# Kernel tuning notes

Measured on AMD Instinct MI355X. Metric: run time of the kernel, lower is better.

The kernel has to match this reference:

```python
import jax, jax.numpy as jnp
import numpy as np

B, D_IN, D_H = 8192, 1024, 1024

def setup_inputs() -> dict:
    key = jax.random.key(0)
    ks = jax.random.split(key, 20)
    s_in = 1.0 / np.sqrt(D_IN)
    s_h = 1.0 / np.sqrt(D_H)
    inp = {
        'input': jax.random.normal(ks[0], (B, D_IN), jnp.float32),
        'h_0': jax.random.normal(ks[1], (B, D_H), jnp.float32),
        'c_0': jax.random.normal(ks[2], (B, D_H), jnp.float32),
    }
    names = ['i', 'f', 'g', 'o']
    for idx, g in enumerate(names):
        inp[f'W_{g}_i2h'] = jax.random.uniform(ks[3 + 4 * idx], (D_H, D_IN), jnp.float32, -s_in, s_in)
        inp[f'b_{g}_i2h'] = jax.random.uniform(ks[4 + 4 * idx], (D_H,), jnp.float32, -s_in, s_in)
        inp[f'W_{g}_h2h'] = jax.random.uniform(ks[5 + 4 * idx], (D_H, D_H), jnp.float32, -s_h, s_h)
        inp[f'b_{g}_h2h'] = jax.random.uniform(ks[6 + 4 * idx], (D_H,), jnp.float32, -s_h, s_h)
    return inp


def reference(input, h_0, c_0,
              W_i_i2h, b_i_i2h, W_i_h2h, b_i_h2h,
              W_f_i2h, b_f_i2h, W_f_h2h, b_f_h2h,
              W_g_i2h, b_g_i2h, W_g_h2h, b_g_h2h,
              W_o_i2h, b_o_i2h, W_o_h2h, b_o_h2h):
    # pre-activations: x @ W_i2h^T + b + h @ W_h2h^T + b  (Linear uses y = x W^T + b)
    def lin(x, W, b):
        return x @ W.T + b
    it = jax.nn.sigmoid(lin(input, W_i_i2h, b_i_i2h) + lin(h_0, W_i_h2h, b_i_h2h))
    ft = jax.nn.sigmoid(lin(input, W_f_i2h, b_f_i2h) + lin(h_0, W_f_h2h, b_f_h2h))
    ot = jax.nn.sigmoid(lin(input, W_o_i2h, b_o_i2h) + lin(h_0, W_o_h2h, b_o_h2h))
    gt = jnp.tanh(lin(input, W_g_i2h, b_g_i2h) + lin(h_0, W_g_h2h, b_g_h2h))
    ct = ft * c_0 + it * gt
    output = ot * jnp.tanh(ct)
    return (output, ct)
```

## Files before the change

### kernel.cpp

```cpp
#include <hip/hip_runtime.h>
#include <cstdint>

typedef __attribute__((ext_vector_type(8))) short bf16x8;
typedef __attribute__((ext_vector_type(4))) float f32x4;
typedef __attribute__((ext_vector_type(4))) unsigned short u16x4;
typedef __attribute__((ext_vector_type(8))) unsigned short u16x8;

typedef __attribute__((address_space(1))) unsigned int gu32_t;
typedef __attribute__((address_space(3))) unsigned int lu32_t;

#define BATCH 8192
#define DIN 1024
#define DH 1024
#define KD 2048
#define ND 4096

__device__ __forceinline__ unsigned short f2bf(float f) {
    union { float f; unsigned int u; } v; v.f = f;
    unsigned int u = v.u;
    u += 0x7fffu + ((u >> 16) & 1u);
    return (unsigned short)(u >> 16);
}
__device__ __forceinline__ float bf2f(unsigned short s) {
    union { unsigned int u; float f; } v; v.u = ((unsigned int)s) << 16;
    return v.f;
}
__device__ __forceinline__ float sigmoidf_(float x) {
    return 1.0f / (1.0f + __expf(-x));
}
__device__ __forceinline__ float tanhf_(float x) {
    float xc = fminf(fmaxf(x, -15.0f), 15.0f);
    float e2 = __expf(2.0f * xc);
    return (e2 - 1.0f) / (e2 + 1.0f);
}

__global__ void __launch_bounds__(256) convert_A(const float* __restrict__ x,
                                                 const float* __restrict__ h,
                                                 unsigned short* __restrict__ A) {
    const int t = blockIdx.x * 256 + threadIdx.x;
    const int64_t off = (int64_t)t * 8;
    const int row = (int)(off >> 11);
    const int k = (int)(off & 2047);
    const float* src = (k < DIN) ? (x + (int64_t)row * DIN + k)
                                 : (h + (int64_t)row * DH + (k - DIN));
    f32x4 v0 = *(const f32x4*)src;
    f32x4 v1 = *(const f32x4*)(src + 4);
    u16x8 o;
    o[0] = f2bf(v0[0]); o[1] = f2bf(v0[1]); o[2] = f2bf(v0[2]); o[3] = f2bf(v0[3]);
    o[4] = f2bf(v1[0]); o[5] = f2bf(v1[1]); o[6] = f2bf(v1[2]); o[7] = f2bf(v1[3]);
    *(u16x8*)(A + off) = o;
}

__global__ void __launch_bounds__(256) convert_B(
        const float* __restrict__ Wii, const float* __restrict__ Wih,
        const float* __restrict__ Wfi, const float* __restrict__ Wfh,
        const float* __restrict__ Wgi, const float* __restrict__ Wgh,
        const float* __restrict__ Woi, const float* __restrict__ Woh,
        unsigned short* __restrict__ B) {
    const int t = blockIdx.x * 256 + threadIdx.x;
    const int64_t off = (int64_t)t * 8;
    const int brow = (int)(off >> 11);
    const int k = (int)(off & 2047);
    const int gate = brow >> 10;
    const int n = brow & 1023;
    const float* Wi2h = (gate == 0) ? Wii : (gate == 1) ? Wfi : (gate == 2) ? Wgi : Woi;
    const float* Wh2h = (gate == 0) ? Wih : (gate == 1) ? Wfh : (gate == 2) ? Wgh : Woh;
    const float* src = (k < 1024) ? (Wi2h + (int64_t)n * 1024 + k)
                                  : (Wh2h + (int64_t)n * 1024 + (k - 1024));
    f32x4 v0 = *(const f32x4*)src;
    f32x4 v1 = *(const f32x4*)(src + 4);
    u16x8 o;
    o[0] = f2bf(v0[0]); o[1] = f2bf(v0[1]); o[2] = f2bf(v0[2]); o[3] = f2bf(v0[3]);
    o[4] = f2bf(v1[0]); o[5] = f2bf(v1[1]); o[6] = f2bf(v1[2]); o[7] = f2bf(v1[3]);
    *(u16x8*)(B + off) = o;
}

__global__ void __launch_bounds__(256) gemm_preact(
        const unsigned short* __restrict__ A,
        const unsigned short* __restrict__ Bw,
        unsigned short* __restrict__ C) {
    __shared__ __align__(16) unsigned short ldsA[128 * 32];
    __shared__ __align__(16) unsigned short ldsB[128 * 32];

    const int bid = blockIdx.x;
    const int swz = ((bid & 7) << 8) | (bid >> 3);
    const int bm = swz >> 5;
    const int bn = swz & 31;
    const int t = threadIdx.x;
    const int lane = t & 63;
    const int wave = t >> 6;
    const int wm = (wave >> 1) << 6;
    const int wn = (wave & 1) << 6;

    f32x4 acc[4][4];
#pragma unroll
    for (int m = 0; m < 4; ++m)
#pragma unroll
        for (int n = 0; n < 4; ++n)
            acc[m][n] = (f32x4){0.f, 0.f, 0.f, 0.f};

    const int c0i = t;
    const int c1i = t + 256;
    const int64_t aOff0 = (int64_t)(bm * 128 + (c0i >> 2)) * KD + ((c0i & 3) << 3);
    const int64_t aOff1 = (int64_t)(bm * 128 + (c1i >> 2)) * KD + ((c1i & 3) << 3);
    const int64_t bOff0 = (int64_t)(bn * 128 + (c0i >> 2)) * KD + ((c0i & 3) << 3);
    const int64_t bOff1 = (int64_t)(bn * 128 + (c1i >> 2)) * KD + ((c1i & 3) << 3);
    unsigned short* lA0 = &ldsA[wave * 512];
    unsigned short* lA1 = &ldsA[2048 + wave * 512];
    unsigned short* lB0 = &ldsB[wave * 512];
    unsigned short* lB1 = &ldsB[2048 + wave * 512];

    const int r = lane & 15;
    const int kq = (lane >> 4) << 3;

    for (int k0 = 0; k0 < KD; k0 += 32) {
        __syncthreads();
        __builtin_amdgcn_global_load_lds((const gu32_t*)(A + aOff0 + k0), (lu32_t*)lA0, 16, 0, 0);
        __builtin_amdgcn_global_load_lds((const gu32_t*)(A + aOff1 + k0), (lu32_t*)lA1, 16, 0, 0);
        __builtin_amdgcn_global_load_lds((const gu32_t*)(Bw + bOff0 + k0), (lu32_t*)lB0, 16, 0, 0);
        __builtin_amdgcn_global_load_lds((const gu32_t*)(Bw + bOff1 + k0), (lu32_t*)lB1, 16, 0, 0);
        __syncthreads();

        bf16x8 af[4], bfr[4];
#pragma unroll
        for (int m = 0; m < 4; ++m)
            af[m] = *(const bf16x8*)&ldsA[(wm + m * 16 + r) * 32 + kq];
#pragma unroll
        for (int n = 0; n < 4; ++n)
            bfr[n] = *(const bf16x8*)&ldsB[(wn + n * 16 + r) * 32 + kq];
#pragma unroll
        for (int m = 0; m < 4; ++m)
#pragma unroll
            for (int n = 0; n < 4; ++n)
                acc[m][n] = __builtin_amdgcn_mfma_f32_16x16x32_bf16(af[m], bfr[n], acc[m][n], 0, 0, 0);
    }

    const int colBase = bn * 128 + wn + r;
    const int rowBase = bm * 128 + wm + ((lane >> 4) << 2);
#pragma unroll
    for (int m = 0; m < 4; ++m)
#pragma unroll
        for (int n = 0; n < 4; ++n) {
            const int col = colBase + n * 16;
#pragma unroll
            for (int j = 0; j < 4; ++j) {
                const int row = rowBase + m * 16 + j;
                C[(int64_t)row * ND + col] = f2bf(acc[m][n][j]);
            }
        }
}

__global__ void __launch_bounds__(256) lstm_epilogue(
        const unsigned short* __restrict__ C,
        const float* __restrict__ c0,
        const float* __restrict__ bii, const float* __restrict__ bih,
        const float* __restrict__ bfi, const float* __restrict__ bfh,
        const float* __restrict__ bgi, const float* __restrict__ bgh,
        const float* __restrict__ boi, const float* __restrict__ boh,
        float* __restrict__ out) {
    const int t = blockIdx.x * 256 + threadIdx.x;
    const int64_t e = (int64_t)t * 4;
    const int n = (int)(e & 1023);
    const int64_t cb = ((e >> 10) << 12) | n;
    u16x4 pi = *(const u16x4*)&C[cb];
    u16x4 pf = *(const u16x4*)&C[cb + 1024];
    u16x4 pg = *(const u16x4*)&C[cb + 2048];
    u16x4 po = *(const u16x4*)&C[cb + 3072];
    f32x4 cv = *(const f32x4*)&c0[e];
    f32x4 b_i0 = *(const f32x4*)&bii[n], b_i1 = *(const f32x4*)&bih[n];
    f32x4 b_f0 = *(const f32x4*)&bfi[n], b_f1 = *(const f32x4*)&bfh[n];
    f32x4 b_g0 = *(const f32x4*)&bgi[n], b_g1 = *(const f32x4*)&bgh[n];
    f32x4 b_o0 = *(const f32x4*)&boi[n], b_o1 = *(const f32x4*)&boh[n];
    f32x4 ov, ctv;
#pragma unroll
    for (int j = 0; j < 4; ++j) {
        float it = sigmoidf_(bf2f(pi[j]) + b_i0[j] + b_i1[j]);
        float ft = sigmoidf_(bf2f(pf[j]) + b_f0[j] + b_f1[j]);
        float gt = tanhf_(bf2f(pg[j]) + b_g0[j] + b_g1[j]);
        float ot = sigmoidf_(bf2f(po[j]) + b_o0[j] + b_o1[j]);
        float ct = ft * cv[j] + it * gt;
        ctv[j] = ct;
        ov[j] = ot * tanhf_(ct);
    }
    *(f32x4*)&out[e] = ov;
    *(f32x4*)&out[(int64_t)BATCH * DH + e] = ctv;
}

extern "C" void kernel_launch(void* const* d_in, const int* in_sizes, int n_in,
                              void* d_out, int out_size, void* d_ws, size_t ws_size,
                              hipStream_t stream) {
    const float* x   = (const float*)d_in[0];
    const float* h0  = (const float*)d_in[1];
    const float* c0  = (const float*)d_in[2];
    const float* Wii = (const float*)d_in[3];
    const float* bii = (const float*)d_in[4];
    const float* Wih = (const float*)d_in[5];
    const float* bih = (const float*)d_in[6];
    const float* Wfi = (const float*)d_in[7];
    const float* bfi = (const float*)d_in[8];
    const float* Wfh = (const float*)d_in[9];
    const float* bfh = (const float*)d_in[10];
    const float* Wgi = (const float*)d_in[11];
    const float* bgi = (const float*)d_in[12];
    const float* Wgh = (const float*)d_in[13];
    const float* bgh = (const float*)d_in[14];
    const float* Woi = (const float*)d_in[15];
    const float* boi = (const float*)d_in[16];
    const float* Woh = (const float*)d_in[17];
    const float* boh = (const float*)d_in[18];

    unsigned short* A  = (unsigned short*)d_ws;
    unsigned short* Bw = A + (size_t)BATCH * KD;
    unsigned short* C  = Bw + (size_t)ND * KD;
    float* out = (float*)d_out;

    convert_A<<<8192, 256, 0, stream>>>(x, h0, A);
    convert_B<<<4096, 256, 0, stream>>>(Wii, Wih, Wfi, Wfh, Wgi, Wgh, Woi, Woh, Bw);
    gemm_preact<<<2048, 256, 0, stream>>>(A, Bw, C);
    lstm_epilogue<<<8192, 256, 0, stream>>>(C, c0, bii, bih, bfi, bfh, bgi, bgh, boi, boh, out);
}
```

Baseline: 379.1 us.

## Fuse LSTM epilogue into GEMM with gate-interleaved weights and merged conversion kernel

Weight rows are reordered so the four gates for each hidden unit sit next to each other in N. Each GEMM tile can then compute the LSTM cell directly, staging its accumulators through LDS and writing h and c without the bf16 preactivation buffer. The two conversion kernels are merged into one that also precomputes summed biases, cutting launches and the round trip of an 8192x4096 intermediate. The cost is an added LDS-staged epilogue with extra barriers and more LDS per block, which may lower occupancy.

After: 406.5 us. 1.07x slower.

```diff
diff --git a/kernel.cpp b/kernel.cpp
--- a/kernel.cpp
+++ b/kernel.cpp
@@ -3,7 +3,6 @@
 
 typedef __attribute__((ext_vector_type(8))) short bf16x8;
 typedef __attribute__((ext_vector_type(4))) float f32x4;
-typedef __attribute__((ext_vector_type(4))) unsigned short u16x4;
 typedef __attribute__((ext_vector_type(8))) unsigned short u16x8;
 
 typedef __attribute__((address_space(1))) unsigned int gu32_t;
@@ -21,10 +20,6 @@
     u += 0x7fffu + ((u >> 16) & 1u);
     return (unsigned short)(u >> 16);
 }
-__device__ __forceinline__ float bf2f(unsigned short s) {
-    union { unsigned int u; float f; } v; v.u = ((unsigned int)s) << 16;
-    return v.f;
-}
 __device__ __forceinline__ float sigmoidf_(float x) {
     return 1.0f / (1.0f + __expf(-x));
 }
@@ -34,53 +29,71 @@
     return (e2 - 1.0f) / (e2 + 1.0f);
 }
 
-__global__ void __launch_bounds__(256) convert_A(const float* __restrict__ x,
-                                                 const float* __restrict__ h,
-                                                 unsigned short* __restrict__ A) {
-    const int t = blockIdx.x * 256 + threadIdx.x;
-    const int64_t off = (int64_t)t * 8;
-    const int row = (int)(off >> 11);
-    const int k = (int)(off & 2047);
-    const float* src = (k < DIN) ? (x + (int64_t)row * DIN + k)
-                                 : (h + (int64_t)row * DH + (k - DIN));
-    f32x4 v0 = *(const f32x4*)src;
-    f32x4 v1 = *(const f32x4*)(src + 4);
-    u16x8 o;
-    o[0] = f2bf(v0[0]); o[1] = f2bf(v0[1]); o[2] = f2bf(v0[2]); o[3] = f2bf(v0[3]);
-    o[4] = f2bf(v1[0]); o[5] = f2bf(v1[1]); o[6] = f2bf(v1[2]); o[7] = f2bf(v1[3]);
-    *(u16x8*)(A + off) = o;
-}
-
-__global__ void __launch_bounds__(256) convert_B(
+__global__ void __launch_bounds__(256) convert_all(
+        const float* __restrict__ x, const float* __restrict__ h,
         const float* __restrict__ Wii, const float* __restrict__ Wih,
         const float* __restrict__ Wfi, const float* __restrict__ Wfh,
         const float* __restrict__ Wgi, const float* __restrict__ Wgh,
         const float* __restrict__ Woi, const float* __restrict__ Woh,
-        unsigned short* __restrict__ B) {
+        const float* __restrict__ bii, const float* __restrict__ bih,
+        const float* __restrict__ bfi, const float* __restrict__ bfh,
+        const float* __restrict__ bgi, const float* __restrict__ bgh,
+        const float* __restrict__ boi, const float* __restrict__ boh,
+        unsigned short* __restrict__ A, unsigned short* __restrict__ B,
+        float* __restrict__ bsum) {
     const int t = blockIdx.x * 256 + threadIdx.x;
-    const int64_t off = (int64_t)t * 8;
-    const int brow = (int)(off >> 11);
-    const int k = (int)(off & 2047);
-    const int gate = brow >> 10;
-    const int n = brow & 1023;
-    const float* Wi2h = (gate == 0) ? Wii : (gate == 1) ? Wfi : (gate == 2) ? Wgi : Woi;
-    const float* Wh2h = (gate == 0) ? Wih : (gate == 1) ? Wfh : (gate == 2) ? Wgh : Woh;
-    const float* src = (k < 1024) ? (Wi2h + (int64_t)n * 1024 + k)
-                                  : (Wh2h + (int64_t)n * 1024 + (k - 1024));
-    f32x4 v0 = *(const f32x4*)src;
-    f32x4 v1 = *(const f32x4*)(src + 4);
-    u16x8 o;
-    o[0] = f2bf(v0[0]); o[1] = f2bf(v0[1]); o[2] = f2bf(v0[2]); o[3] = f2bf(v0[3]);
-    o[4] = f2bf(v1[0]); o[5] = f2bf(v1[1]); o[6] = f2bf(v1[2]); o[7] = f2bf(v1[3]);
-    *(u16x8*)(B + off) = o;
-}
-
-__global__ void __launch_bounds__(256) gemm_preact(
+    if (t < 2097152) {
+        const int64_t off = (int64_t)t * 8;
+        const int row = (int)(off >> 11);
+        const int k = (int)(off & 2047);
+        const float* src = (k < DIN) ? (x + (int64_t)row * DIN + k)
+                                     : (h + (int64_t)row * DH + (k - DIN));
+        f32x4 v0 = *(const f32x4*)src;
+        f32x4 v1 = *(const f32x4*)(src + 4);
+        u16x8 o;
+        o[0] = f2bf(v0[0]); o[1] = f2bf(v0[1]); o[2] = f2bf(v0[2]); o[3] = f2bf(v0[3]);
+        o[4] = f2bf(v1[0]); o[5] = f2bf(v1[1]); o[6] = f2bf(v1[2]); o[7] = f2bf(v1[3]);
+        *(u16x8*)(A + off) = o;
+    } else if (t < 3145728) {
+        const int tb = t - 2097152;
+        const int64_t off = (int64_t)tb * 8;
+        const int brow = (int)(off >> 11);
+        const int k = (int)(off & 2047);
+        const int gate = brow & 3;
+        const int n = brow >> 2;
+        const float* Wi2h = (gate == 0) ? Wii : (gate == 1) ? Wfi : (gate == 2) ? Wgi : Woi;
+        const float* Wh2h = (gate == 0) ? Wih : (gate == 1) ? Wfh : (gate == 2) ? Wgh : Woh;
+        const float* src = (k < 1024) ? (Wi2h + (int64_t)n * 1024 + k)
+                                      : (Wh2h + (int64_t)n * 1024 + (k - 1024));
+        f32x4 v0 = *(const f32x4*)src;
+        f32x4 v1 = *(const f32x4*)(src + 4);
+        u16x8 o;
+        o[0] = f2bf(v0[0]); o[1] = f2bf(v0[1]); o[2] = f2bf(v0[2]); o[3] = f2bf(v0[3]);
+        o[4] = f2bf(v1[0]); o[5] = f2bf(v1[1]); o[6] = f2bf(v1[2]); o[7] = f2bf(v1[3]);
+        *(u16x8*)(B + off) = o;
+    } else {
+        const int b = t - 3145728;
+#pragma unroll
+        for (int i = 0; i < 8; ++i) {
+            const int e = b * 8 + i;
+            const int n = e >> 2;
+            const int g = e & 3;
+            const float* bi = (g == 0) ? bii : (g == 1) ? bfi : (g == 2) ? bgi : boi;
+            const float* bh = (g == 0) ? bih : (g == 1) ? bfh : (g == 2) ? bgh : boh;
+            bsum[e] = bi[n] + bh[n];
+        }
+    }
+}
+
+__global__ void __launch_bounds__(256) gemm_lstm(
         const unsigned short* __restrict__ A,
         const unsigned short* __restrict__ Bw,
-        unsigned short* __restrict__ C) {
+        const float* __restrict__ c0,
+        const float* __restrict__ bsum,
+        float* __restrict__ out) {
     __shared__ __align__(16) unsigned short ldsA[128 * 32];
     __shared__ __align__(16) unsigned short ldsB[128 * 32];
+    __shared__ __align__(16) float preLds[64][128];
 
     const int bid = blockIdx.x;
     const int swz = ((bid & 7) << 8) | (bid >> 3);
@@ -135,55 +148,51 @@
                 acc[m][n] = __builtin_amdgcn_mfma_f32_16x16x32_bf16(af[m], bfr[n], acc[m][n], 0, 0, 0);
     }
 
-    const int colBase = bn * 128 + wn + r;
-    const int rowBase = bm * 128 + wm + ((lane >> 4) << 2);
-#pragma unroll
-    for (int m = 0; m < 4; ++m)
-#pragma unroll
-        for (int n = 0; n < 4; ++n) {
-            const int col = colBase + n * 16;
+    f32x4 bs[4];
+#pragma unroll
+    for (int i = 0; i < 4; ++i)
+        bs[i] = *(const f32x4*)&bsum[bn * 128 + (t & 7) * 16 + i * 4];
+
+    const int rq = (lane >> 4) << 2;
+
+#pragma unroll
+    for (int c = 0; c < 2; ++c) {
+        __syncthreads();
+        if (wm == c * 64) {
+#pragma unroll
+            for (int m = 0; m < 4; ++m)
+#pragma unroll
+                for (int n = 0; n < 4; ++n)
+#pragma unroll
+                    for (int j = 0; j < 4; ++j)
+                        preLds[m * 16 + rq + j][wn + n * 16 + r] = acc[m][n][j];
+        }
+        __syncthreads();
+#pragma unroll
+        for (int p = 0; p < 2; ++p) {
+            const int lr = p * 32 + (t >> 3);
+            const int R = bm * 128 + c * 64 + lr;
+            f32x4 pr[4];
+#pragma unroll
+            for (int i = 0; i < 4; ++i)
+                pr[i] = *(const f32x4*)&preLds[lr][(t & 7) * 16 + i * 4];
+            const int64_t eo = (int64_t)R * DH + bn * 32 + (t & 7) * 4;
+            f32x4 cv = *(const f32x4*)&c0[eo];
+            f32x4 hv, ctv;
 #pragma unroll
             for (int j = 0; j < 4; ++j) {
-                const int row = rowBase + m * 16 + j;
-                C[(int64_t)row * ND + col] = f2bf(acc[m][n][j]);
+                float it = sigmoidf_(pr[j][0] + bs[j][0]);
+                float ft = sigmoidf_(pr[j][1] + bs[j][1]);
+                float gt = tanhf_(pr[j][2] + bs[j][2]);
+                float ot = sigmoidf_(pr[j][3] + bs[j][3]);
+                float ct = ft * cv[j] + it * gt;
+                ctv[j] = ct;
+                hv[j] = ot * tanhf_(ct);
             }
+            *(f32x4*)&out[eo] = hv;
+            *(f32x4*)&out[(int64_t)BATCH * DH + eo] = ctv;
         }
-}
-
-__global__ void __launch_bounds__(256) lstm_epilogue(
-        const unsigned short* __restrict__ C,
-        const float* __restrict__ c0,
-        const float* __restrict__ bii, const float* __restrict__ bih,
-        const float* __restrict__ bfi, const float* __restrict__ bfh,
-        const float* __restrict__ bgi, const float* __restrict__ bgh,
-        const float* __restrict__ boi, const float* __restrict__ boh,
-        float* __restrict__ out) {
-    const int t = blockIdx.x * 256 + threadIdx.x;
-    const int64_t e = (int64_t)t * 4;
-    const int n = (int)(e & 1023);
-    const int64_t cb = ((e >> 10) << 12) | n;
-    u16x4 pi = *(const u16x4*)&C[cb];
-    u16x4 pf = *(const u16x4*)&C[cb + 1024];
-    u16x4 pg = *(const u16x4*)&C[cb + 2048];
-    u16x4 po = *(const u16x4*)&C[cb + 3072];
-    f32x4 cv = *(const f32x4*)&c0[e];
-    f32x4 b_i0 = *(const f32x4*)&bii[n], b_i1 = *(const f32x4*)&bih[n];
-    f32x4 b_f0 = *(const f32x4*)&bfi[n], b_f1 = *(const f32x4*)&bfh[n];
-    f32x4 b_g0 = *(const f32x4*)&bgi[n], b_g1 = *(const f32x4*)&bgh[n];
-    f32x4 b_o0 = *(const f32x4*)&boi[n], b_o1 = *(const f32x4*)&boh[n];
-    f32x4 ov, ctv;
-#pragma unroll
-    for (int j = 0; j < 4; ++j) {
-        float it = sigmoidf_(bf2f(pi[j]) + b_i0[j] + b_i1[j]);
-        float ft = sigmoidf_(bf2f(pf[j]) + b_f0[j] + b_f1[j]);
-        float gt = tanhf_(bf2f(pg[j]) + b_g0[j] + b_g1[j]);
-        float ot = sigmoidf_(bf2f(po[j]) + b_o0[j] + b_o1[j]);
-        float ct = ft * cv[j] + it * gt;
-        ctv[j] = ct;
-        ov[j] = ot * tanhf_(ct);
     }
-    *(f32x4*)&out[e] = ov;
-    *(f32x4*)&out[(int64_t)BATCH * DH + e] = ctv;
 }
 
 extern "C" void kernel_launch(void* const* d_in, const int* in_sizes, int n_in,
@@ -211,11 +220,12 @@
 
     unsigned short* A  = (unsigned short*)d_ws;
     unsigned short* Bw = A + (size_t)BATCH * KD;
-    unsigned short* C  = Bw + (size_t)ND * KD;
+    float* bsum = (float*)(Bw + (size_t)ND * KD);
     float* out = (float*)d_out;
 
-    convert_A<<<8192, 256, 0, stream>>>(x, h0, A);
-    convert_B<<<4096, 256, 0, stream>>>(Wii, Wih, Wfi, Wfh, Wgi, Wgh, Woi, Woh, Bw);
-    gemm_preact<<<2048, 256, 0, stream>>>(A, Bw, C);
-    lstm_epilogue<<<8192, 256, 0, stream>>>(C, c0, bii, bih, bfi, bfh, bgi, bgh, boi, boh, out);
-}
+    convert_all<<<12290, 256, 0, stream>>>(x, h0,
+        Wii, Wih, Wfi, Wfh, Wgi, Wgh, Woi, Woh,
+        bii, bih, bfi, bfh, bgi, bgh, boi, boh,
+        A, Bw, bsum);
+    gemm_lstm<<<2048, 256, 0, stream>>>(A, Bw, c0, bsum, out);
+}
```
